# Kernel tuning notes

Measured on AMD Instinct MI355X. Metric: run time of the kernel, lower is better.

## Reference

```python
import jax, jax.numpy as jnp
import numpy as np

N_VAR = 1_000_000
N_CON = 500_000
N_EDGE = 8_000_000
H = 10  # n_h_feats


def setup_inputs() -> dict:
    key = jax.random.key(0)
    ks = jax.random.split(key, 20)
    f32 = jnp.float32
    s = 0.3  # weight init scale
    return {
        'var_c': jax.random.normal(ks[0], (N_VAR,), f32),
        'var_x': jax.random.normal(ks[1], (N_VAR,), f32),
        'con_b': jax.random.normal(ks[2], (N_CON,), f32),
        'edge_src': jax.random.randint(ks[3], (N_EDGE,), 0, N_VAR, jnp.int32),
        'edge_dst': jax.random.randint(ks[4], (N_EDGE,), 0, N_CON, jnp.int32),
        'edge_w': jax.random.uniform(ks[5], (N_EDGE,), f32),
        'Wv': jax.random.normal(ks[6], (2, H), f32) * s,
        'bv': jnp.zeros((H,), f32),
        'Wc': jax.random.normal(ks[7], (1, H), f32) * s,
        'bc': jnp.zeros((H,), f32),
        'W1': jax.random.normal(ks[8], (H, H), f32) * s,
        'b1': jnp.zeros((H,), f32),
        'W2': jax.random.normal(ks[9], (H, H), f32) * s,
        'b2': jnp.zeros((H,), f32),
        'Wo1': jax.random.normal(ks[10], (H, H), f32) * s,
        'bo1': jnp.zeros((H,), f32),
        'Wo2': jax.random.normal(ks[11], (H, H), f32) * s,
        'bo2': jnp.zeros((H,), f32),
        'Wo3': jax.random.normal(ks[12], (H, 1), f32) * s,
        'bo3': jnp.zeros((1,), f32),
    }


def _graph_conv(feat_src, src, dst, w, n_dst, deg_src, deg_dst, W, b):
    # DGL GraphConv, norm='both', with edge weights:
    # h = D_src^{-1/2} x ; m_e = h[src_e] * w_e ; agg = scatter_sum(m, dst)
    # out = (D_dst^{-1/2} agg) @ W + b
    h = feat_src * jax.lax.rsqrt(deg_src)[:, None]
    m = h[src] * w[:, None]                      # [E, H] gather + scale
    agg = jax.ops.segment_sum(m, dst, num_segments=n_dst)  # scatter-add
    agg = agg * jax.lax.rsqrt(deg_dst)[:, None]
    return agg @ W + b


def reference(var_c, var_x, con_b, edge_src, edge_dst, edge_w,
              Wv, bv, Wc, bc, W1, b1, W2, b2, Wo1, bo1, Wo2, bo2, Wo3, bo3):
    # node embeddings
    var_feat = jnp.stack([var_c, var_x], axis=1)            # [N_VAR, 2]
    con_feat = con_b.reshape(-1, 1)                          # [N_CON, 1]
    X_var = jax.nn.relu(var_feat @ Wv + bv)                  # [N_VAR, H]
    X_con = jax.nn.relu(con_feat @ Wc + bc)                  # computed in original; unused by GraphConv (no dst-feat term)

    ones_e = jnp.ones((edge_src.shape[0],), jnp.float32)
    deg_var = jnp.maximum(jax.ops.segment_sum(ones_e, edge_src, num_segments=N_VAR), 1.0)
    deg_con = jnp.maximum(jax.ops.segment_sum(ones_e, edge_dst, num_segments=N_CON), 1.0)

    # conv1['con'] is overwritten by conv2['con'] in the original (v2c src feats are X_var both times)
    h_con = jax.nn.relu(_graph_conv(X_var, edge_src, edge_dst, edge_w, N_CON, deg_var, deg_con, W2, b2))
    # likewise conv1['var'] is overwritten by conv2['var'] (c2v src feats are h_con both times)
    h_var = jax.nn.relu(_graph_conv(h_con, edge_dst, edge_src, edge_w, N_VAR, deg_con, deg_var, W2, b2))

    z = jax.nn.relu(h_var @ Wo1 + bo1)
    z = jax.nn.relu(z @ Wo2 + bo2)
    logit = z @ Wo3 + bo3                                    # [N_VAR, 1]
    # dgl.readout_nodes(op='mean') over a single batched graph
    return jnp.mean(logit, axis=0, keepdims=True)            # [1, 1]
```

## Files before the change

### kernel.cpp

```cpp
#include <hip/hip_runtime.h>

#define NVAR 1000000
#define NCON 500000
#define EPB 8192
#define FCAP 4480


__global__ __launch_bounds__(256) void kA_hist2(const int4* __restrict__ src4,
                                                const int4* __restrict__ dst4,
                                                unsigned* __restrict__ bhV,
                                                unsigned* __restrict__ bhC,
                                                int ne4, int nblk) {
    __shared__ unsigned hv[1024], hc[1024];
    int tid = threadIdx.x, b = blockIdx.x;
    for (int t = tid; t < 1024; t += 256) { hv[t] = 0; hc[t] = 0; }
    __syncthreads();
    int beg = b * (EPB / 4), end = min(ne4, beg + (EPB / 4));
    for (int i = beg + tid; i < end; i += 256) {
        int4 s = src4[i];
        int4 d = dst4[i];
        atomicAdd(&hv[s.x >> 10], 1u); atomicAdd(&hv[s.y >> 10], 1u);
        atomicAdd(&hv[s.z >> 10], 1u); atomicAdd(&hv[s.w >> 10], 1u);
        atomicAdd(&hc[d.x >> 9], 1u);  atomicAdd(&hc[d.y >> 9], 1u);
        atomicAdd(&hc[d.z >> 9], 1u);  atomicAdd(&hc[d.w >> 9], 1u);
    }
    __syncthreads();
    for (int t = tid; t < 1024; t += 256) {
        bhV[(size_t)t * nblk + b] = hv[t];
        bhC[(size_t)t * nblk + b] = hc[t];
    }
}

__global__ __launch_bounds__(256) void kA_scat(const int* __restrict__ keys,
                                               const int* __restrict__ vals,
                                               const float* __restrict__ w,
                                               const unsigned int* __restrict__ scanned,
                                               int2* __restrict__ bucketed,
                                               int ne, int shift, int nblk) {
    __shared__ unsigned int h[1024];
    __shared__ unsigned int lb[1024];
    __shared__ unsigned int gb[1024];
    __shared__ unsigned int sc[256];
    __shared__ int2 stage[EPB];
    int tid = threadIdx.x, b = blockIdx.x;
    for (int t = tid; t < 1024; t += 256) {
        h[t] = 0;
        gb[t] = scanned[(size_t)t * nblk + b];
    }
    __syncthreads();
    int beg = b * EPB, end = min(ne, beg + EPB), cnt = end - beg;
    int cnt4 = cnt >> 2;
    const int4* keys4 = (const int4*)(keys + beg);
    for (int i = tid; i < cnt4; i += 256) {
        int4 k = keys4[i];
        atomicAdd(&h[k.x >> shift], 1u);
        atomicAdd(&h[k.y >> shift], 1u);
        atomicAdd(&h[k.z >> shift], 1u);
        atomicAdd(&h[k.w >> shift], 1u);
    }
    for (int i = cnt4 * 4 + tid; i < cnt; i += 256) atomicAdd(&h[keys[beg + i] >> shift], 1u);
    __syncthreads();
    unsigned v0, v1, v2, v3;
    int q = tid * 4;
    v0 = h[q]; v1 = h[q + 1]; v2 = h[q + 2]; v3 = h[q + 3];
    sc[tid] = v0 + v1 + v2 + v3;
    __syncthreads();
    for (int dd = 1; dd < 256; dd <<= 1) {
        unsigned add = (tid >= dd) ? sc[tid - dd] : 0u;
        __syncthreads();
        sc[tid] += add;
        __syncthreads();
    }
    unsigned ex = (tid == 0) ? 0u : sc[tid - 1];
    lb[q]     = ex;
    lb[q + 1] = ex + v0;
    lb[q + 2] = ex + v0 + v1;
    lb[q + 3] = ex + v0 + v1 + v2;
    __syncthreads();
    for (int t = tid; t < 1024; t += 256) h[t] = 0;
    __syncthreads();
    unsigned mask = (1u << shift) - 1u;
    const int4* vals4 = (const int4*)(vals + beg);
    const float4* w4 = (const float4*)(w + beg);
    for (int i = tid; i < cnt4; i += 256) {
        int4 k = keys4[i];
        int4 v = vals4[i];
        float4 ww = w4[i];
        {
            unsigned bkt = (unsigned)k.x >> shift;
            unsigned r = atomicAdd(&h[bkt], 1u);
            stage[lb[bkt] + r] = make_int2(__float_as_int(ww.x),
                                           (v.x << shift) | (unsigned)(k.x & (int)mask));
        }
        {
            unsigned bkt = (unsigned)k.y >> shift;
            unsigned r = atomicAdd(&h[bkt], 1u);
            stage[lb[bkt] + r] = make_int2(__float_as_int(ww.y),
                                           (v.y << shift) | (unsigned)(k.y & (int)mask));
        }
        {
            unsigned bkt = (unsigned)k.z >> shift;
            unsigned r = atomicAdd(&h[bkt], 1u);
            stage[lb[bkt] + r] = make_int2(__float_as_int(ww.z),
                                           (v.z << shift) | (unsigned)(k.z & (int)mask));
        }
        {
            unsigned bkt = (unsigned)k.w >> shift;
            unsigned r = atomicAdd(&h[bkt], 1u);
            stage[lb[bkt] + r] = make_int2(__float_as_int(ww.w),
                                           (v.w << shift) | (unsigned)(k.w & (int)mask));
        }
    }
    for (int i = cnt4 * 4 + tid; i < cnt; i += 256) {
        int k = keys[beg + i];
        unsigned bkt = (unsigned)k >> shift;
        unsigned r = atomicAdd(&h[bkt], 1u);
        stage[lb[bkt] + r] = make_int2(__float_as_int(w[beg + i]),
                                       (vals[beg + i] << shift) | (unsigned)(k & (int)mask));
    }
    __syncthreads();
    for (int i = tid; i < cnt; i += 256) {
        unsigned bb = 0;
#pragma unroll
        for (int step = 512; step > 0; step >>= 1) {
            unsigned cand = bb + step;
            if (cand < 1024 && lb[cand] <= (unsigned)i) bb = cand;
        }
        bucketed[gb[bb] + ((unsigned)i - lb[bb])] = stage[i];
    }
}

__global__ __launch_bounds__(256) void kDeg(const int2* __restrict__ bucketed,
                                            const unsigned* __restrict__ scanned,
                                            unsigned* __restrict__ deg,
                                            int nnodes, int nblk, int lowbits) {
    __shared__ unsigned h[1024];
    int d = blockIdx.x, tid = threadIdx.x;
    int W = 1 << lowbits;
    unsigned mask = (unsigned)(W - 1);
    unsigned base = scanned[(size_t)d * nblk], next = scanned[(size_t)(d + 1) * nblk];
    for (int t = tid; t < W; t += 256) h[t] = 0;
    __syncthreads();
    for (unsigned i = base + tid; i < next; i += 256)
        atomicAdd(&h[(unsigned)bucketed[i].y & mask], 1u);
    __syncthreads();
    int lo = d << lowbits;
    for (int t = tid; t < W; t += 256) {
        int node = lo + t;
        if (node < nnodes) deg[node] = h[t];
    }
}

__global__ __launch_bounds__(256) void k_scan_blocks(const unsigned int* in,
                                                     unsigned int* out,
                                                     unsigned int* bsum,
                                                     int n) {
    __shared__ unsigned int sT[256];
    int base = blockIdx.x * 1024 + threadIdx.x * 4;
    unsigned int v0 = 0, v1 = 0, v2 = 0, v3 = 0;
    if (base + 3 < n) {
        uint4 u = *(const uint4*)(in + base);
        v0 = u.x; v1 = u.y; v2 = u.z; v3 = u.w;
    } else {
        if (base     < n) v0 = in[base];
        if (base + 1 < n) v1 = in[base + 1];
        if (base + 2 < n) v2 = in[base + 2];
        if (base + 3 < n) v3 = in[base + 3];
    }
    sT[threadIdx.x] = v0 + v1 + v2 + v3;
    __syncthreads();
    for (int d = 1; d < 256; d <<= 1) {
        unsigned int add = (threadIdx.x >= (unsigned)d) ? sT[threadIdx.x - d] : 0u;
        __syncthreads();
        sT[threadIdx.x] += add;
        __syncthreads();
    }
    unsigned int excl = (threadIdx.x == 0) ? 0u : sT[threadIdx.x - 1];
    if (base     < n) out[base]     = excl;
    if (base + 1 < n) out[base + 1] = excl + v0;
    if (base + 2 < n) out[base + 2] = excl + v0 + v1;
    if (base + 3 < n) out[base + 3] = excl + v0 + v1 + v2;
    if (threadIdx.x == 255 && bsum) bsum[blockIdx.x] = sT[255];
}

__global__ __launch_bounds__(256) void k_scan_add(unsigned int* __restrict__ data,
                                                  const unsigned int* __restrict__ bscan,
                                                  int n) {
    int base = blockIdx.x * 1024 + threadIdx.x * 4;
    unsigned int add = bscan[blockIdx.x];
    if (base + 3 < n) {
        uint4 u = *(const uint4*)(data + base);
        u.x += add; u.y += add; u.z += add; u.w += add;
        *(uint4*)(data + base) = u;
    } else {
        if (base     < n) data[base]     += add;
        if (base + 1 < n) data[base + 1] += add;
        if (base + 2 < n) data[base + 2] += add;
        if (base + 3 < n) data[base + 3] += add;
    }
}


__global__ __launch_bounds__(256) void k_xvar_p(const float* __restrict__ var_c,
                                                const float* __restrict__ var_x,
                                                const unsigned int* __restrict__ deg_var,
                                                const float* __restrict__ Wv,
                                                const float* __restrict__ bv,
                                                float* __restrict__ Xs, int n) {
    int i = blockIdx.x * blockDim.x + threadIdx.x;
    if (i >= n) return;
    float c = var_c[i], x = var_x[i];
    float rs = rsqrtf(fmaxf((float)deg_var[i], 1.0f));
    float o[16];
#pragma unroll
    for (int j = 0; j < 10; j++) {
        float t = fmaf(c, Wv[j], fmaf(x, Wv[10 + j], bv[j]));
        o[j] = fmaxf(t, 0.0f) * rs;
    }
#pragma unroll
    for (int j = 10; j < 16; j++) o[j] = 0.0f;
    float4* dst4 = (float4*)(Xs + (size_t)i * 16);
#pragma unroll
    for (int j = 0; j < 4; j++)
        dst4[j] = make_float4(o[4 * j], o[4 * j + 1], o[4 * j + 2], o[4 * j + 3]);
}

#define GATHER4(eA, eB, eC, eD, TAB)                                          \
    {                                                                         \
        float4 v0 = *(const float4*)(TAB + (size_t)(eA).y * 16 + c0);         \
        float4 v1 = *(const float4*)(TAB + (size_t)(eB).y * 16 + c0);         \
        float4 v2 = *(const float4*)(TAB + (size_t)(eC).y * 16 + c0);         \
        float4 v3 = *(const float4*)(TAB + (size_t)(eD).y * 16 + c0);         \
        float w0 = __int_as_float((eA).x), w1 = __int_as_float((eB).x);       \
        float w2 = __int_as_float((eC).x), w3 = __int_as_float((eD).x);       \
        acc.x = fmaf(w0, v0.x, acc.x); acc.y = fmaf(w0, v0.y, acc.y);         \
        acc.z = fmaf(w0, v0.z, acc.z); acc.w = fmaf(w0, v0.w, acc.w);         \
        acc.x = fmaf(w1, v1.x, acc.x); acc.y = fmaf(w1, v1.y, acc.y);         \
        acc.z = fmaf(w1, v1.z, acc.z); acc.w = fmaf(w1, v1.w, acc.w);         \
        acc.x = fmaf(w2, v2.x, acc.x); acc.y = fmaf(w2, v2.y, acc.y);         \
        acc.z = fmaf(w2, v2.z, acc.z); acc.w = fmaf(w2, v2.w, acc.w);         \
        acc.x = fmaf(w3, v3.x, acc.x); acc.y = fmaf(w3, v3.y, acc.y);         \
        acc.z = fmaf(w3, v3.z, acc.z); acc.w = fmaf(w3, v3.w, acc.w);         \
    }

__global__ __launch_bounds__(512) void kF_con(const int2* __restrict__ bucketed,
                                              const unsigned* __restrict__ scanned,
                                              const unsigned* __restrict__ startC,
                                              const float* __restrict__ Xs,
                                              const float* __restrict__ W2,
                                              const float* __restrict__ b2,
                                              float* __restrict__ hs, int nblk, int netot) {
    __shared__ unsigned sraw[257], cr[256];
    __shared__ float sW[100], sb[10];
    __shared__ int2 stage[FCAP];
    int tid = threadIdx.x;
    int d = blockIdx.x >> 1, half = blockIdx.x & 1;
    int gbase = (d << 9) + half * 256;
    for (int t = tid; t < 100; t += 512) sW[t] = W2[t];
    if (tid < 10) sb[tid] = b2[tid];
    for (int t = tid; t < 257; t += 512) {
        int g = gbase + t;
        sraw[t] = (g < NCON) ? startC[g] : (unsigned)netot;
    }
    if (tid < 256) cr[tid] = 0;
    __syncthreads();
    unsigned own_beg = sraw[0], own_end = sraw[256];
    bool fit = (int)(own_end - own_beg) <= FCAP;
    unsigned bbase = scanned[(size_t)d * nblk];
    unsigned bnext = scanned[(size_t)(d + 1) * nblk];
    int bsz = (int)(bnext - bbase);
    if (fit) {
        for (int i = tid; i < bsz; i += 512) {
            int2 p = bucketed[bbase + i];
            unsigned low = (unsigned)p.y & 511u;
            if ((int)(low >> 8) == half) {
                unsigned nl = low & 255u;
                unsigned r = atomicAdd(&cr[nl], 1u);
                stage[sraw[nl] - own_beg + r] = make_int2(p.x, p.y >> 9);
            }
        }
    }
    __syncthreads();
    int quad = tid >> 2, lane = tid & 3, c0 = lane * 4;
#pragma unroll
    for (int rr = 0; rr < 2; rr++) {
        int nl = rr * 128 + quad;
        int g = gbase + nl;
        if (g >= NCON) continue;
        float4 acc = make_float4(0.f, 0.f, 0.f, 0.f);
        unsigned cnt;
        if (fit) {
            unsigned beg = sraw[nl] - own_beg;
            cnt = cr[nl];
            unsigned end = beg + cnt, p = beg;
            for (; p + 4 <= end; p += 4) {
                int2 e0 = stage[p], e1 = stage[p + 1], e2 = stage[p + 2], e3 = stage[p + 3];
                GATHER4(e0, e1, e2, e3, Xs);
            }
            for (; p < end; ++p) {
                int2 e = stage[p];
                float4 v = *(const float4*)(Xs + (size_t)e.y * 16 + c0);
                float we = __int_as_float(e.x);
                acc.x = fmaf(we, v.x, acc.x); acc.y = fmaf(we, v.y, acc.y);
                acc.z = fmaf(we, v.z, acc.z); acc.w = fmaf(we, v.w, acc.w);
            }
        } else {
            cnt = 0;
            unsigned target = (unsigned)(half * 256 + nl);
            for (int i = 0; i < bsz; ++i) {
                int2 p = bucketed[bbase + i];
                if (((unsigned)p.y & 511u) == target) {
                    ++cnt;
                    float4 v = *(const float4*)(Xs + (size_t)((unsigned)p.y >> 9) * 16 + c0);
                    float we = __int_as_float(p.x);
                    acc.x = fmaf(we, v.x, acc.x); acc.y = fmaf(we, v.y, acc.y);
                    acc.z = fmaf(we, v.z, acc.z); acc.w = fmaf(we, v.w, acc.w);
                }
            }
        }
        float rs = rsqrtf(fmaxf((float)cnt, 1.0f));
        float a[10];
        a[0] = __shfl(acc.x, 0, 4); a[1] = __shfl(acc.y, 0, 4);
        a[2] = __shfl(acc.z, 0, 4); a[3] = __shfl(acc.w, 0, 4);
        a[4] = __shfl(acc.x, 1, 4); a[5] = __shfl(acc.y, 1, 4);
        a[6] = __shfl(acc.z, 1, 4); a[7] = __shfl(acc.w, 1, 4);
        a[8] = __shfl(acc.x, 2, 4); a[9] = __shfl(acc.y, 2, 4);
#pragma unroll
        for (int j = 0; j < 10; j++) a[j] *= rs;
        float o[12];
#pragma unroll
        for (int k = 0; k < 10; k++) {
            float t = sb[k];
#pragma unroll
            for (int j = 0; j < 10; j++) t = fmaf(a[j], sW[j * 10 + k], t);
            o[k] = fmaxf(t, 0.0f) * rs;
        }
        o[10] = 0.0f; o[11] = 0.0f;
        float4 wv = (lane < 3) ? make_float4(o[c0], o[c0 + 1], o[c0 + 2], o[c0 + 3])
                               : make_float4(0.f, 0.f, 0.f, 0.f);
        *(float4*)(hs + (size_t)g * 16 + c0) = wv;
    }
}

__global__ __launch_bounds__(512) void kF_fin(const int2* __restrict__ bucketed,
                                              const unsigned* __restrict__ scanned,
                                              const unsigned* __restrict__ startV,
                                              const float* __restrict__ feat,
                                              const float* __restrict__ W2,
                                              const float* __restrict__ b2,
                                              const float* __restrict__ Wo1,
                                              const float* __restrict__ bo1,
                                              const float* __restrict__ Wo2,
                                              const float* __restrict__ bo2,
                                              const float* __restrict__ Wo3,
                                              const float* __restrict__ bo3,
                                              double* __restrict__ partials, int nblk, int netot) {
    __shared__ unsigned sraw[513], cr[512];
    __shared__ float sW2[100], sb2[10], sWo1[100], sbo1[10], sWo2[100], sbo2[10], sWo3[10], sbo3v;
    __shared__ int2 stage[FCAP];
    __shared__ double red[512];
    int tid = threadIdx.x;
    int d = blockIdx.x >> 1, half = blockIdx.x & 1;
    int gbase = (d << 10) + half * 512;
    for (int t = tid; t < 100; t += 512) { sW2[t] = W2[t]; sWo1[t] = Wo1[t]; sWo2[t] = Wo2[t]; }
    if (tid < 10) {
        sb2[tid] = b2[tid]; sbo1[tid] = bo1[tid]; sbo2[tid] = bo2[tid]; sWo3[tid] = Wo3[tid];
    }
    if (tid == 0) sbo3v = bo3[0];
    for (int t = tid; t < 513; t += 512) {
        int g = gbase + t;
        sraw[t] = (g < NVAR) ? startV[g] : (unsigned)netot;
    }
    cr[tid] = 0;
    __syncthreads();
    unsigned own_beg = sraw[0], own_end = sraw[512];
    bool fit = (int)(own_end - own_beg) <= FCAP;
    unsigned bbase = scanned[(size_t)d * nblk];
    unsigned bnext = scanned[(size_t)(d + 1) * nblk];
    int bsz = (int)(bnext - bbase);
    if (fit) {
        for (int i = tid; i < bsz; i += 512) {
            int2 p = bucketed[bbase + i];
            unsigned low = (unsigned)p.y & 1023u;
            if ((int)(low >> 9) == half) {
                unsigned nl = low & 511u;
                unsigned r = atomicAdd(&cr[nl], 1u);
                stage[sraw[nl] - own_beg + r] = make_int2(p.x, p.y >> 10);
            }
        }
    }
    __syncthreads();
    int quad = tid >> 2, lane = tid & 3, c0 = lane * 4;
    double accd = 0.0;
#pragma unroll
    for (int rr = 0; rr < 4; rr++) {
        int nl = rr * 128 + quad;
        int g = gbase + nl;
        if (g >= NVAR) continue;
        float4 acc = make_float4(0.f, 0.f, 0.f, 0.f);
        unsigned cnt;
        if (fit) {
            unsigned beg = sraw[nl] - own_beg;
            cnt = cr[nl];
            unsigned end = beg + cnt, p = beg;
            for (; p + 4 <= end; p += 4) {
                int2 e0 = stage[p], e1 = stage[p + 1], e2 = stage[p + 2], e3 = stage[p + 3];
                GATHER4(e0, e1, e2, e3, feat);
            }
            for (; p < end; ++p) {
                int2 e = stage[p];
                float4 v = *(const float4*)(feat + (size_t)e.y * 16 + c0);
                float we = __int_as_float(e.x);
                acc.x = fmaf(we, v.x, acc.x); acc.y = fmaf(we, v.y, acc.y);
                acc.z = fmaf(we, v.z, acc.z); acc.w = fmaf(we, v.w, acc.w);
            }
        } else {
            cnt = 0;
            unsigned target = (unsigned)(half * 512 + nl);
            for (int i = 0; i < bsz; ++i) {
                int2 p = bucketed[bbase + i];
                if (((unsigned)p.y & 1023u) == target) {
                    ++cnt;
                    float4 v = *(const float4*)(feat + (size_t)((unsigned)p.y >> 10) * 16 + c0);
                    float we = __int_as_float(p.x);
                    acc.x = fmaf(we, v.x, acc.x); acc.y = fmaf(we, v.y, acc.y);
                    acc.z = fmaf(we, v.z, acc.z); acc.w = fmaf(we, v.w, acc.w);
                }
            }
        }
        float rs = rsqrtf(fmaxf((float)cnt, 1.0f));
        float a[10];
        a[0] = __shfl(acc.x, 0, 4); a[1] = __shfl(acc.y, 0, 4);
        a[2] = __shfl(acc.z, 0, 4); a[3] = __shfl(acc.w, 0, 4);
        a[4] = __shfl(acc.x, 1, 4); a[5] = __shfl(acc.y, 1, 4);
        a[6] = __shfl(acc.z, 1, 4); a[7] = __shfl(acc.w, 1, 4);
        a[8] = __shfl(acc.x, 2, 4); a[9] = __shfl(acc.y, 2, 4);
#pragma unroll
        for (int j = 0; j < 10; j++) a[j] *= rs;
        float hh[10], z[10];
#pragma unroll
        for (int k = 0; k < 10; k++) {
            float t = sb2[k];
#pragma unroll
            for (int j = 0; j < 10; j++) t = fmaf(a[j], sW2[j * 10 + k], t);
            hh[k] = fmaxf(t, 0.0f);
        }
#pragma unroll
        for (int k = 0; k < 10; k++) {
            float t = sbo1[k];
#pragma unroll
            for (int j = 0; j < 10; j++) t = fmaf(hh[j], sWo1[j * 10 + k], t);
            z[k] = fmaxf(t, 0.0f);
        }
        float t3 = sbo3v;
#pragma unroll
        for (int k = 0; k < 10; k++) {
            float t = sbo2[k];
#pragma unroll
            for (int j = 0; j < 10; j++) t = fmaf(z[j], sWo2[j * 10 + k], t);
            t = fmaxf(t, 0.0f);
            t3 = fmaf(t, sWo3[k], t3);
        }
        if (lane == 0) accd += (double)t3;
    }
    red[tid] = accd;
    __syncthreads();
    for (int off = 256; off > 0; off >>= 1) {
        if (tid < off) red[tid] += red[tid + off];
        __syncthreads();
    }
    if (tid == 0) partials[blockIdx.x] = red[0];
}

__global__ __launch_bounds__(256) void k_out(const double* __restrict__ partials, int np,
                                             float* __restrict__ out) {
    __shared__ double red[256];
    double a = 0.0;
    for (int i = threadIdx.x; i < np; i += blockDim.x) a += partials[i];
    red[threadIdx.x] = a;
    __syncthreads();
    for (int off = 128; off > 0; off >>= 1) {
        if (threadIdx.x < off) red[threadIdx.x] += red[threadIdx.x + off];
        __syncthreads();
    }
    if (threadIdx.x == 0) out[0] = (float)(red[0] / (double)NVAR);
}


extern "C" void kernel_launch(void* const* d_in, const int* in_sizes, int n_in,
                              void* d_out, int out_size, void* d_ws, size_t ws_size,
                              hipStream_t stream) {
    const float* var_c  = (const float*)d_in[0];
    const float* var_x  = (const float*)d_in[1];
    const int*   e_src  = (const int*)d_in[3];
    const int*   e_dst  = (const int*)d_in[4];
    const float* e_w    = (const float*)d_in[5];
    const float* Wv     = (const float*)d_in[6];
    const float* bv     = (const float*)d_in[7];
    const float* W2     = (const float*)d_in[12];
    const float* b2     = (const float*)d_in[13];
    const float* Wo1    = (const float*)d_in[14];
    const float* bo1    = (const float*)d_in[15];
    const float* Wo2    = (const float*)d_in[16];
    const float* bo2    = (const float*)d_in[17];
    const float* Wo3    = (const float*)d_in[18];
    const float* bo3    = (const float*)d_in[19];
    float* out = (float*)d_out;
    const int ne = in_sizes[3];
    (void)n_in; (void)out_size; (void)ws_size;

    const int B = 256;
    const int nblkA = (ne + EPB - 1) / EPB;
    const int scanN = 1024 * nblkA;
    const int NBs   = (scanN + 1023) / 1024;
    const int BKV   = (NVAR + 1023) >> 10;
    const int BKC   = (NCON + 511) >> 9;
    const int NBV   = (NVAR + 1023) / 1024;
    const int NBC   = (NCON + 1023) / 1024;
    const int ne4   = ne / 4;

    char* ws = (char*)d_ws;
    size_t off = 0;
    auto walloc = [&](size_t bytes) {
        void* p = ws + off;
        off = (off + bytes + 255) & ~(size_t)255;
        return p;
    };

    int2*     bucketedV = (int2*)walloc((size_t)ne * 8);
    int2*     bucketedC = (int2*)walloc((size_t)ne * 8);
    float*    Xs64      = (float*)walloc((size_t)NVAR * 16 * 4);
    float*    hs64      = (float*)walloc((size_t)NCON * 16 * 4);
    unsigned* scannedV  = (unsigned*)walloc((size_t)scanN * 4);
    unsigned* scannedC  = (unsigned*)walloc((size_t)scanN * 4);
    unsigned* bhV       = (unsigned*)walloc((size_t)scanN * 4);
    unsigned* bhC       = (unsigned*)walloc((size_t)scanN * 4);
    unsigned* bsumA     = (unsigned*)walloc(4096);
    unsigned* bscanA    = (unsigned*)walloc(4096);
    unsigned* bdummy    = (unsigned*)walloc(256);
    double*   partials  = (double*)walloc((size_t)(BKV * 2) * 8 + 64);
    unsigned* deg_var   = bhV;
    unsigned* deg_con   = bhC;

    kA_hist2<<<nblkA, B, 0, stream>>>((const int4*)e_src, (const int4*)e_dst,
                                      bhV, bhC, ne4, nblkA);

    k_scan_blocks<<<NBs, B, 0, stream>>>(bhV, scannedV, bsumA, scanN);
    k_scan_blocks<<<1,   B, 0, stream>>>(bsumA, bscanA, bdummy, NBs);
    k_scan_add   <<<NBs, B, 0, stream>>>(scannedV, bscanA, scanN);
    k_scan_blocks<<<NBs, B, 0, stream>>>(bhC, scannedC, bsumA, scanN);
    k_scan_blocks<<<1,   B, 0, stream>>>(bsumA, bscanA, bdummy, NBs);
    k_scan_add   <<<NBs, B, 0, stream>>>(scannedC, bscanA, scanN);

    kA_scat<<<nblkA, B, 0, stream>>>(e_src, e_dst, e_w, scannedV, bucketedV, ne, 10, nblkA);

    kDeg<<<BKV, B, 0, stream>>>(bucketedV, scannedV, deg_var, NVAR, nblkA, 10);

    k_xvar_p<<<(NVAR + B - 1) / B, B, 0, stream>>>(var_c, var_x, deg_var, Wv, bv, Xs64, NVAR);

    k_scan_blocks<<<NBV, B, 0, stream>>>(deg_var, deg_var, bsumA, NVAR);
    k_scan_blocks<<<1,   B, 0, stream>>>(bsumA, bscanA, bdummy, NBV);
    k_scan_add   <<<NBV, B, 0, stream>>>(deg_var, bscanA, NVAR);

    kA_scat<<<nblkA, B, 0, stream>>>(e_dst, e_src, e_w, scannedC, bucketedC, ne, 9, nblkA);

    kDeg<<<BKC, B, 0, stream>>>(bucketedC, scannedC, deg_con, NCON, nblkA, 9);
    k_scan_blocks<<<NBC, B, 0, stream>>>(deg_con, deg_con, bsumA, NCON);
    k_scan_blocks<<<1,   B, 0, stream>>>(bsumA, bscanA, bdummy, NBC);
    k_scan_add   <<<NBC, B, 0, stream>>>(deg_con, bscanA, NCON);

    kF_con<<<BKC * 2, 512, 0, stream>>>(bucketedC, scannedC, deg_con, Xs64, W2, b2,
                                        hs64, nblkA, ne);

    kF_fin<<<BKV * 2, 512, 0, stream>>>(bucketedV, scannedV, deg_var, hs64, W2, b2,
                                        Wo1, bo1, Wo2, bo2, Wo3, bo3, partials, nblkA, ne);

    k_out<<<1, B, 0, stream>>>(partials, BKV * 2, out);
}
```

Before: 585.5 us.

## Fuse variable embedding into constraint gather and halve edges per block

Instead of materializing a 64-byte padded embedding per variable, a 16-byte (c, x, rsqrt deg) record is packed and the constraint-side gather recomputes relu(Wv·feat+bv)·rs per edge. This shrinks the written table and the random-gather traffic by 4x at the cost of extra FMAs per edge. EPB is halved to 4096, which doubles the number of histogram and scatter blocks. Because the block-sum arrays grow, a single-block looping scan kernel (k_scan_mid) replaces the one-block scan of block sums.

```diff
diff --git a/kernel.cpp b/kernel.cpp
--- a/kernel.cpp
+++ b/kernel.cpp
@@ -2,7 +2,7 @@
 
 #define NVAR 1000000
 #define NCON 500000
-#define EPB 8192
+#define EPB 4096
 #define FCAP 4480
 
 
@@ -183,6 +183,31 @@
     if (threadIdx.x == 255 && bsum) bsum[blockIdx.x] = sT[255];
 }
 
+__global__ __launch_bounds__(256) void k_scan_mid(const unsigned* __restrict__ in,
+                                                  unsigned* __restrict__ out, int n) {
+    __shared__ unsigned sT[256];
+    __shared__ unsigned carry;
+    if (threadIdx.x == 0) carry = 0;
+    __syncthreads();
+    for (int base = 0; base < n; base += 256) {
+        int i = base + threadIdx.x;
+        unsigned v = (i < n) ? in[i] : 0u;
+        sT[threadIdx.x] = v;
+        __syncthreads();
+        for (int d = 1; d < 256; d <<= 1) {
+            unsigned add = (threadIdx.x >= (unsigned)d) ? sT[threadIdx.x - d] : 0u;
+            __syncthreads();
+            sT[threadIdx.x] += add;
+            __syncthreads();
+        }
+        unsigned excl = carry + ((threadIdx.x == 0) ? 0u : sT[threadIdx.x - 1]);
+        if (i < n) out[i] = excl;
+        __syncthreads();
+        if (threadIdx.x == 255) carry += sT[255];
+        __syncthreads();
+    }
+}
+
 __global__ __launch_bounds__(256) void k_scan_add(unsigned int* __restrict__ data,
                                                   const unsigned int* __restrict__ bscan,
                                                   int n) {
@@ -201,28 +226,177 @@
 }
 
 
-__global__ __launch_bounds__(256) void k_xvar_p(const float* __restrict__ var_c,
-                                                const float* __restrict__ var_x,
-                                                const unsigned int* __restrict__ deg_var,
-                                                const float* __restrict__ Wv,
-                                                const float* __restrict__ bv,
-                                                float* __restrict__ Xs, int n) {
+__global__ __launch_bounds__(256) void k_pack(const float* __restrict__ var_c,
+                                              const float* __restrict__ var_x,
+                                              const unsigned int* __restrict__ deg_var,
+                                              float4* __restrict__ vcr, int n) {
     int i = blockIdx.x * blockDim.x + threadIdx.x;
     if (i >= n) return;
-    float c = var_c[i], x = var_x[i];
     float rs = rsqrtf(fmaxf((float)deg_var[i], 1.0f));
-    float o[16];
-#pragma unroll
-    for (int j = 0; j < 10; j++) {
-        float t = fmaf(c, Wv[j], fmaf(x, Wv[10 + j], bv[j]));
-        o[j] = fmaxf(t, 0.0f) * rs;
-    }
-#pragma unroll
-    for (int j = 10; j < 16; j++) o[j] = 0.0f;
-    float4* dst4 = (float4*)(Xs + (size_t)i * 16);
-#pragma unroll
-    for (int j = 0; j < 4; j++)
-        dst4[j] = make_float4(o[4 * j], o[4 * j + 1], o[4 * j + 2], o[4 * j + 3]);
+    vcr[i] = make_float4(var_c[i], var_x[i], rs, 0.0f);
+}
+
+#define EMBADD(e)                                                             \
+    {                                                                         \
+        float4 vv = vcr[(size_t)(e).y];                                       \
+        float we = __int_as_float((e).x);                                     \
+        float t0 = fmaf(vv.x, wv0[0], fmaf(vv.y, wv1[0], bvr[0]));            \
+        float t1 = fmaf(vv.x, wv0[1], fmaf(vv.y, wv1[1], bvr[1]));            \
+        float t2 = fmaf(vv.x, wv0[2], fmaf(vv.y, wv1[2], bvr[2]));            \
+        float t3 = fmaf(vv.x, wv0[3], fmaf(vv.y, wv1[3], bvr[3]));            \
+        acc.x = fmaf(we, fmaxf(t0, 0.f) * vv.z, acc.x);                       \
+        acc.y = fmaf(we, fmaxf(t1, 0.f) * vv.z, acc.y);                       \
+        acc.z = fmaf(we, fmaxf(t2, 0.f) * vv.z, acc.z);                       \
+        acc.w = fmaf(we, fmaxf(t3, 0.f) * vv.z, acc.w);                       \
+    }
+
+#define EMB4(eA, eB, eC, eD)                                                  \
+    {                                                                         \
+        float4 vA = vcr[(size_t)(eA).y];                                      \
+        float4 vB = vcr[(size_t)(eB).y];                                      \
+        float4 vC = vcr[(size_t)(eC).y];                                      \
+        float4 vD = vcr[(size_t)(eD).y];                                      \
+        float wA = __int_as_float((eA).x), wB = __int_as_float((eB).x);       \
+        float wC = __int_as_float((eC).x), wD = __int_as_float((eD).x);       \
+        float t0, t1, t2, t3;                                                 \
+        t0 = fmaf(vA.x, wv0[0], fmaf(vA.y, wv1[0], bvr[0]));                  \
+        t1 = fmaf(vA.x, wv0[1], fmaf(vA.y, wv1[1], bvr[1]));                  \
+        t2 = fmaf(vA.x, wv0[2], fmaf(vA.y, wv1[2], bvr[2]));                  \
+        t3 = fmaf(vA.x, wv0[3], fmaf(vA.y, wv1[3], bvr[3]));                  \
+        acc.x = fmaf(wA, fmaxf(t0, 0.f) * vA.z, acc.x);                       \
+        acc.y = fmaf(wA, fmaxf(t1, 0.f) * vA.z, acc.y);                       \
+        acc.z = fmaf(wA, fmaxf(t2, 0.f) * vA.z, acc.z);                       \
+        acc.w = fmaf(wA, fmaxf(t3, 0.f) * vA.z, acc.w);                       \
+        t0 = fmaf(vB.x, wv0[0], fmaf(vB.y, wv1[0], bvr[0]));                  \
+        t1 = fmaf(vB.x, wv0[1], fmaf(vB.y, wv1[1], bvr[1]));                  \
+        t2 = fmaf(vB.x, wv0[2], fmaf(vB.y, wv1[2], bvr[2]));                  \
+        t3 = fmaf(vB.x, wv0[3], fmaf(vB.y, wv1[3], bvr[3]));                  \
+        acc.x = fmaf(wB, fmaxf(t0, 0.f) * vB.z, acc.x);                       \
+        acc.y = fmaf(wB, fmaxf(t1, 0.f) * vB.z, acc.y);                       \
+        acc.z = fmaf(wB, fmaxf(t2, 0.f) * vB.z, acc.z);                       \
+        acc.w = fmaf(wB, fmaxf(t3, 0.f) * vB.z, acc.w);                       \
+        t0 = fmaf(vC.x, wv0[0], fmaf(vC.y, wv1[0], bvr[0]));                  \
+        t1 = fmaf(vC.x, wv0[1], fmaf(vC.y, wv1[1], bvr[1]));                  \
+        t2 = fmaf(vC.x, wv0[2], fmaf(vC.y, wv1[2], bvr[2]));                  \
+        t3 = fmaf(vC.x, wv0[3], fmaf(vC.y, wv1[3], bvr[3]));                  \
+        acc.x = fmaf(wC, fmaxf(t0, 0.f) * vC.z, acc.x);                       \
+        acc.y = fmaf(wC, fmaxf(t1, 0.f) * vC.z, acc.y);                       \
+        acc.z = fmaf(wC, fmaxf(t2, 0.f) * vC.z, acc.z);                       \
+        acc.w = fmaf(wC, fmaxf(t3, 0.f) * vC.z, acc.w);                       \
+        t0 = fmaf(vD.x, wv0[0], fmaf(vD.y, wv1[0], bvr[0]));                  \
+        t1 = fmaf(vD.x, wv0[1], fmaf(vD.y, wv1[1], bvr[1]));                  \
+        t2 = fmaf(vD.x, wv0[2], fmaf(vD.y, wv1[2], bvr[2]));                  \
+        t3 = fmaf(vD.x, wv0[3], fmaf(vD.y, wv1[3], bvr[3]));                  \
+        acc.x = fmaf(wD, fmaxf(t0, 0.f) * vD.z, acc.x);                       \
+        acc.y = fmaf(wD, fmaxf(t1, 0.f) * vD.z, acc.y);                       \
+        acc.z = fmaf(wD, fmaxf(t2, 0.f) * vD.z, acc.z);                       \
+        acc.w = fmaf(wD, fmaxf(t3, 0.f) * vD.z, acc.w);                       \
+    }
+
+__global__ __launch_bounds__(512) void kF_con(const int2* __restrict__ bucketed,
+                                              const unsigned* __restrict__ scanned,
+                                              const unsigned* __restrict__ startC,
+                                              const float4* __restrict__ vcr,
+                                              const float* __restrict__ Wv,
+                                              const float* __restrict__ bv,
+                                              const float* __restrict__ W2,
+                                              const float* __restrict__ b2,
+                                              float* __restrict__ hs, int nblk, int netot) {
+    __shared__ unsigned sraw[257], cr[256];
+    __shared__ float sWv[20], sbv[10], sW[100], sb[10];
+    __shared__ int2 stage[FCAP];
+    int tid = threadIdx.x;
+    int d = blockIdx.x >> 1, half = blockIdx.x & 1;
+    int gbase = (d << 9) + half * 256;
+    for (int t = tid; t < 100; t += 512) sW[t] = W2[t];
+    if (tid < 10) sb[tid] = b2[tid];
+    if (tid < 20) sWv[tid] = Wv[tid];
+    if (tid >= 20 && tid < 30) sbv[tid - 20] = bv[tid - 20];
+    for (int t = tid; t < 257; t += 512) {
+        int g = gbase + t;
+        sraw[t] = (g < NCON) ? startC[g] : (unsigned)netot;
+    }
+    if (tid < 256) cr[tid] = 0;
+    __syncthreads();
+    unsigned own_beg = sraw[0], own_end = sraw[256];
+    bool fit = (int)(own_end - own_beg) <= FCAP;
+    unsigned bbase = scanned[(size_t)d * nblk];
+    unsigned bnext = scanned[(size_t)(d + 1) * nblk];
+    int bsz = (int)(bnext - bbase);
+    if (fit) {
+        for (int i = tid; i < bsz; i += 512) {
+            int2 p = bucketed[bbase + i];
+            unsigned low = (unsigned)p.y & 511u;
+            if ((int)(low >> 8) == half) {
+                unsigned nl = low & 255u;
+                unsigned r = atomicAdd(&cr[nl], 1u);
+                stage[sraw[nl] - own_beg + r] = make_int2(p.x, p.y >> 9);
+            }
+        }
+    }
+    __syncthreads();
+    int quad = tid >> 2, lane = tid & 3, c0 = lane * 4;
+    float wv0[4], wv1[4], bvr[4];
+#pragma unroll
+    for (int k = 0; k < 4; k++) {
+        int j = c0 + k;
+        wv0[k] = (j < 10) ? sWv[j] : 0.f;
+        wv1[k] = (j < 10) ? sWv[10 + j] : 0.f;
+        bvr[k] = (j < 10) ? sbv[j] : 0.f;
+    }
+#pragma unroll
+    for (int rr = 0; rr < 2; rr++) {
+        int nl = rr * 128 + quad;
+        int g = gbase + nl;
+        if (g >= NCON) continue;
+        float4 acc = make_float4(0.f, 0.f, 0.f, 0.f);
+        unsigned cnt;
+        if (fit) {
+            unsigned beg = sraw[nl] - own_beg;
+            cnt = cr[nl];
+            unsigned end = beg + cnt, p = beg;
+            for (; p + 4 <= end; p += 4) {
+                int2 e0 = stage[p], e1 = stage[p + 1], e2 = stage[p + 2], e3 = stage[p + 3];
+                EMB4(e0, e1, e2, e3);
+            }
+            for (; p < end; ++p) {
+                int2 e = stage[p];
+                EMBADD(e);
+            }
+        } else {
+            cnt = 0;
+            unsigned target = (unsigned)(half * 256 + nl);
+            for (int i = 0; i < bsz; ++i) {
+                int2 p = bucketed[bbase + i];
+                if (((unsigned)p.y & 511u) == target) {
+                    ++cnt;
+                    int2 e = make_int2(p.x, p.y >> 9);
+                    EMBADD(e);
+                }
+            }
+        }
+        float rs = rsqrtf(fmaxf((float)cnt, 1.0f));
+        float a[10];
+        a[0] = __shfl(acc.x, 0, 4); a[1] = __shfl(acc.y, 0, 4);
+        a[2] = __shfl(acc.z, 0, 4); a[3] = __shfl(acc.w, 0, 4);
+        a[4] = __shfl(acc.x, 1, 4); a[5] = __shfl(acc.y, 1, 4);
+        a[6] = __shfl(acc.z, 1, 4); a[7] = __shfl(acc.w, 1, 4);
+        a[8] = __shfl(acc.x, 2, 4); a[9] = __shfl(acc.y, 2, 4);
+#pragma unroll
+        for (int j = 0; j < 10; j++) a[j] *= rs;
+        float o[12];
+#pragma unroll
+        for (int k = 0; k < 10; k++) {
+            float t = sb[k];
+#pragma unroll
+            for (int j = 0; j < 10; j++) t = fmaf(a[j], sW[j * 10 + k], t);
+            o[k] = fmaxf(t, 0.0f) * rs;
+        }
+        o[10] = 0.0f; o[11] = 0.0f;
+        float4 wv = (lane < 3) ? make_float4(o[c0], o[c0 + 1], o[c0 + 2], o[c0 + 3])
+                               : make_float4(0.f, 0.f, 0.f, 0.f);
+        *(float4*)(hs + (size_t)g * 16 + c0) = wv;
+    }
 }
 
 #define GATHER4(eA, eB, eC, eD, TAB)                                          \
@@ -242,105 +416,6 @@
         acc.x = fmaf(w3, v3.x, acc.x); acc.y = fmaf(w3, v3.y, acc.y);         \
         acc.z = fmaf(w3, v3.z, acc.z); acc.w = fmaf(w3, v3.w, acc.w);         \
     }
-
-__global__ __launch_bounds__(512) void kF_con(const int2* __restrict__ bucketed,
-                                              const unsigned* __restrict__ scanned,
-                                              const unsigned* __restrict__ startC,
-                                              const float* __restrict__ Xs,
-                                              const float* __restrict__ W2,
-                                              const float* __restrict__ b2,
-                                              float* __restrict__ hs, int nblk, int netot) {
-    __shared__ unsigned sraw[257], cr[256];
-    __shared__ float sW[100], sb[10];
-    __shared__ int2 stage[FCAP];
-    int tid = threadIdx.x;
-    int d = blockIdx.x >> 1, half = blockIdx.x & 1;
-    int gbase = (d << 9) + half * 256;
-    for (int t = tid; t < 100; t += 512) sW[t] = W2[t];
-    if (tid < 10) sb[tid] = b2[tid];
-    for (int t = tid; t < 257; t += 512) {
-        int g = gbase + t;
-        sraw[t] = (g < NCON) ? startC[g] : (unsigned)netot;
-    }
-    if (tid < 256) cr[tid] = 0;
-    __syncthreads();
-    unsigned own_beg = sraw[0], own_end = sraw[256];
-    bool fit = (int)(own_end - own_beg) <= FCAP;
-    unsigned bbase = scanned[(size_t)d * nblk];
-    unsigned bnext = scanned[(size_t)(d + 1) * nblk];
-    int bsz = (int)(bnext - bbase);
-    if (fit) {
-        for (int i = tid; i < bsz; i += 512) {
-            int2 p = bucketed[bbase + i];
-            unsigned low = (unsigned)p.y & 511u;
-            if ((int)(low >> 8) == half) {
-                unsigned nl = low & 255u;
-                unsigned r = atomicAdd(&cr[nl], 1u);
-                stage[sraw[nl] - own_beg + r] = make_int2(p.x, p.y >> 9);
-            }
-        }
-    }
-    __syncthreads();
-    int quad = tid >> 2, lane = tid & 3, c0 = lane * 4;
-#pragma unroll
-    for (int rr = 0; rr < 2; rr++) {
-        int nl = rr * 128 + quad;
-        int g = gbase + nl;
-        if (g >= NCON) continue;
-        float4 acc = make_float4(0.f, 0.f, 0.f, 0.f);
-        unsigned cnt;
-        if (fit) {
-            unsigned beg = sraw[nl] - own_beg;
-            cnt = cr[nl];
-            unsigned end = beg + cnt, p = beg;
-            for (; p + 4 <= end; p += 4) {
-                int2 e0 = stage[p], e1 = stage[p + 1], e2 = stage[p + 2], e3 = stage[p + 3];
-                GATHER4(e0, e1, e2, e3, Xs);
-            }
-            for (; p < end; ++p) {
-                int2 e = stage[p];
-                float4 v = *(const float4*)(Xs + (size_t)e.y * 16 + c0);
-                float we = __int_as_float(e.x);
-                acc.x = fmaf(we, v.x, acc.x); acc.y = fmaf(we, v.y, acc.y);
-                acc.z = fmaf(we, v.z, acc.z); acc.w = fmaf(we, v.w, acc.w);
-            }
-        } else {
-            cnt = 0;
-            unsigned target = (unsigned)(half * 256 + nl);
-            for (int i = 0; i < bsz; ++i) {
-                int2 p = bucketed[bbase + i];
-                if (((unsigned)p.y & 511u) == target) {
-                    ++cnt;
-                    float4 v = *(const float4*)(Xs + (size_t)((unsigned)p.y >> 9) * 16 + c0);
-                    float we = __int_as_float(p.x);
-                    acc.x = fmaf(we, v.x, acc.x); acc.y = fmaf(we, v.y, acc.y);
-                    acc.z = fmaf(we, v.z, acc.z); acc.w = fmaf(we, v.w, acc.w);
-                }
-            }
-        }
-        float rs = rsqrtf(fmaxf((float)cnt, 1.0f));
-        float a[10];
-        a[0] = __shfl(acc.x, 0, 4); a[1] = __shfl(acc.y, 0, 4);
-        a[2] = __shfl(acc.z, 0, 4); a[3] = __shfl(acc.w, 0, 4);
-        a[4] = __shfl(acc.x, 1, 4); a[5] = __shfl(acc.y, 1, 4);
-        a[6] = __shfl(acc.z, 1, 4); a[7] = __shfl(acc.w, 1, 4);
-        a[8] = __shfl(acc.x, 2, 4); a[9] = __shfl(acc.y, 2, 4);
-#pragma unroll
-        for (int j = 0; j < 10; j++) a[j] *= rs;
-        float o[12];
-#pragma unroll
-        for (int k = 0; k < 10; k++) {
-            float t = sb[k];
-#pragma unroll
-            for (int j = 0; j < 10; j++) t = fmaf(a[j], sW[j * 10 + k], t);
-            o[k] = fmaxf(t, 0.0f) * rs;
-        }
-        o[10] = 0.0f; o[11] = 0.0f;
-        float4 wv = (lane < 3) ? make_float4(o[c0], o[c0 + 1], o[c0 + 2], o[c0 + 3])
-                               : make_float4(0.f, 0.f, 0.f, 0.f);
-        *(float4*)(hs + (size_t)g * 16 + c0) = wv;
-    }
-}
 
 __global__ __launch_bounds__(512) void kF_fin(const int2* __restrict__ bucketed,
                                               const unsigned* __restrict__ scanned,
@@ -529,15 +604,14 @@
 
     int2*     bucketedV = (int2*)walloc((size_t)ne * 8);
     int2*     bucketedC = (int2*)walloc((size_t)ne * 8);
-    float*    Xs64      = (float*)walloc((size_t)NVAR * 16 * 4);
+    float4*   vcr       = (float4*)walloc((size_t)NVAR * 16);
     float*    hs64      = (float*)walloc((size_t)NCON * 16 * 4);
     unsigned* scannedV  = (unsigned*)walloc((size_t)scanN * 4);
     unsigned* scannedC  = (unsigned*)walloc((size_t)scanN * 4);
     unsigned* bhV       = (unsigned*)walloc((size_t)scanN * 4);
     unsigned* bhC       = (unsigned*)walloc((size_t)scanN * 4);
-    unsigned* bsumA     = (unsigned*)walloc(4096);
-    unsigned* bscanA    = (unsigned*)walloc(4096);
-    unsigned* bdummy    = (unsigned*)walloc(256);
+    unsigned* bsumA     = (unsigned*)walloc(8192);
+    unsigned* bscanA    = (unsigned*)walloc(8192);
     double*   partials  = (double*)walloc((size_t)(BKV * 2) * 8 + 64);
     unsigned* deg_var   = bhV;
     unsigned* deg_con   = bhC;
@@ -546,31 +620,31 @@
                                       bhV, bhC, ne4, nblkA);
 
     k_scan_blocks<<<NBs, B, 0, stream>>>(bhV, scannedV, bsumA, scanN);
-    k_scan_blocks<<<1,   B, 0, stream>>>(bsumA, bscanA, bdummy, NBs);
+    k_scan_mid   <<<1,   B, 0, stream>>>(bsumA, bscanA, NBs);
     k_scan_add   <<<NBs, B, 0, stream>>>(scannedV, bscanA, scanN);
     k_scan_blocks<<<NBs, B, 0, stream>>>(bhC, scannedC, bsumA, scanN);
-    k_scan_blocks<<<1,   B, 0, stream>>>(bsumA, bscanA, bdummy, NBs);
+    k_scan_mid   <<<1,   B, 0, stream>>>(bsumA, bscanA, NBs);
     k_scan_add   <<<NBs, B, 0, stream>>>(scannedC, bscanA, scanN);
 
     kA_scat<<<nblkA, B, 0, stream>>>(e_src, e_dst, e_w, scannedV, bucketedV, ne, 10, nblkA);
 
     kDeg<<<BKV, B, 0, stream>>>(bucketedV, scannedV, deg_var, NVAR, nblkA, 10);
 
-    k_xvar_p<<<(NVAR + B - 1) / B, B, 0, stream>>>(var_c, var_x, deg_var, Wv, bv, Xs64, NVAR);
+    k_pack<<<(NVAR + B - 1) / B, B, 0, stream>>>(var_c, var_x, deg_var, vcr, NVAR);
 
     k_scan_blocks<<<NBV, B, 0, stream>>>(deg_var, deg_var, bsumA, NVAR);
-    k_scan_blocks<<<1,   B, 0, stream>>>(bsumA, bscanA, bdummy, NBV);
+    k_scan_mid   <<<1,   B, 0, stream>>>(bsumA, bscanA, NBV);
     k_scan_add   <<<NBV, B, 0, stream>>>(deg_var, bscanA, NVAR);
 
     kA_scat<<<nblkA, B, 0, stream>>>(e_dst, e_src, e_w, scannedC, bucketedC, ne, 9, nblkA);
 
     kDeg<<<BKC, B, 0, stream>>>(bucketedC, scannedC, deg_con, NCON, nblkA, 9);
     k_scan_blocks<<<NBC, B, 0, stream>>>(deg_con, deg_con, bsumA, NCON);
-    k_scan_blocks<<<1,   B, 0, stream>>>(bsumA, bscanA, bdummy, NBC);
+    k_scan_mid   <<<1,   B, 0, stream>>>(bsumA, bscanA, NBC);
     k_scan_add   <<<NBC, B, 0, stream>>>(deg_con, bscanA, NCON);
 
-    kF_con<<<BKC * 2, 512, 0, stream>>>(bucketedC, scannedC, deg_con, Xs64, W2, b2,
-                                        hs64, nblkA, ne);
+    kF_con<<<BKC * 2, 512, 0, stream>>>(bucketedC, scannedC, deg_con, vcr, Wv, bv,
+                                        W2, b2, hs64, nblkA, ne);
 
     kF_fin<<<BKV * 2, 512, 0, stream>>>(bucketedV, scannedV, deg_var, hs64, W2, b2,
                                         Wo1, bo1, Wo2, bo2, Wo3, bo3, partials, nblkA, ne);
```

New measurement: 614.1 us. 1.05x slower.
